# Kernel tuning notes

Hardware: AMD Instinct MI355X
Metric: run time of the kernel (lower is better)

## Reference

```python
import jax, jax.numpy as jnp
import numpy as np

EOS_IDX = 1
B, S, V, E, H = 32, 64, 32000, 512, 512


def _gru_step(x, h, w_ih, w_hh, b_ih, b_hh):
    # PyTorch GRU cell: gates ordered (r, z, n)
    gi = x @ w_ih.T + b_ih
    gh = h @ w_hh.T + b_hh
    i_r, i_z, i_n = jnp.split(gi, 3, axis=-1)
    h_r, h_z, h_n = jnp.split(gh, 3, axis=-1)
    r = jax.nn.sigmoid(i_r + h_r)
    z = jax.nn.sigmoid(i_z + h_z)
    n = jnp.tanh(i_n + r * h_n)
    return (1.0 - z) * n + z * h


def setup_inputs() -> dict:
    key = jax.random.key(0)
    ks = jax.random.split(key, 16)
    u = lambda k, shape: jax.random.uniform(k, shape, jnp.float32, -1.0, 1.0) / np.sqrt(H)
    return {
        "targets": jax.random.randint(ks[0], (B, S), 0, V),
        "targets_kws": jax.random.randint(ks[1], (B, S), 0, V),
        "sent_state": jax.random.normal(ks[2], (1, B, H), jnp.float32),
        "targets_len": jax.random.randint(ks[3], (B,), 1, S),
        "emb": jax.random.normal(ks[4], (V, E), jnp.float32) * 0.05,
        "w_ih_w": u(ks[5], (3 * H, 2 * E)),
        "w_hh_w": u(ks[6], (3 * H, H)),
        "b_ih_w": u(ks[7], (3 * H,)),
        "b_hh_w": u(ks[8], (3 * H,)),
        "w_ih_s": u(ks[9], (3 * H, H)),
        "w_hh_s": u(ks[10], (3 * H, H)),
        "b_ih_s": u(ks[11], (3 * H,)),
        "b_hh_s": u(ks[12], (3 * H,)),
        "out_w": u(ks[13], (V, H)),
        "out_b": u(ks[14], (V,)),
    }


def reference(targets, targets_kws, sent_state, targets_len,
              emb, w_ih_w, w_hh_w, b_ih_w, b_hh_w,
              w_ih_s, w_hh_s, b_ih_s, b_hh_s, out_w, out_b):
    seq = targets.shape[1]
    h0 = sent_state[0]  # nlayers = 1 -> (B, H)
    last_words = targets[:, :-1].T   # (S-1, B)
    keywords = targets_kws[:, 1:].T  # (S-1, B)
    next_words = targets[:, 1:].T    # (S-1, B)

    def step(carry, inp):
        word_h, sent_h = carry
        lw, kw, nw = inp
        x = jnp.concatenate([emb[kw], emb[lw]], axis=-1)  # (B, 2E)
        word_h = _gru_step(x, word_h, w_ih_w, w_hh_w, b_ih_w, b_hh_w)
        logp = jax.nn.log_softmax(word_h @ out_w.T + out_b, axis=-1)
        m = (nw == EOS_IDX).astype(word_h.dtype)[:, None]  # EOS mask
        tmp = _gru_step(word_h, sent_h, w_ih_s, w_hh_s, b_ih_s, b_hh_s)
        sent_h2 = sent_h * (1.0 - m) + tmp * m
        word_h2 = word_h * (1.0 - m) + tmp * m
        return (word_h2, sent_h2), logp

    _, logps = jax.lax.scan(step, (h0, h0), (last_words, keywords, next_words))
    # logps: (S-1, B, V). Masked NLL as in mask_loss().
    tok_logp = jnp.take_along_axis(logps, next_words[:, :, None], axis=2)[:, :, 0]
    valid = (targets_len[None, :] > jnp.arange(1, seq)[:, None]).astype(logps.dtype)
    return -(tok_logp * valid).sum()
```

## Files before the change

### kernel.cpp

```cpp
#include <hip/hip_runtime.h>
#include <stdint.h>

typedef short bf16x8 __attribute__((ext_vector_type(8)));
typedef float f32x4 __attribute__((ext_vector_type(4)));
typedef unsigned short u16;
typedef unsigned long long u64;

#define B_  32
#define S_  64
#define V_  32000
#define H_  512
#define T_  63
#define R_  2016
#define RP_ 2048
#define G3_ 1536
#define NWG 32

#define o_X      0ull
#define o_Wih    4194304ull
#define o_OutW   7340032ull
#define o_PackHH 40108032ull
#define o_PackIS 41680896ull
#define o_PackHS 43253760ull
#define o_GI     44826624ull
#define o_WHf    57212928ull
#define o_WHb    61341696ull
#define o_HPUB   63438848ull
#define o_SPUB   63504384ull
#define o_ARR    63569920ull
#define o_PART   63733760ull
#define o_LSE    72122368ull
#define o_RL     72130560ull
#define o_FLG    72138752ull

__device__ __forceinline__ u16 f2b(float f) {
  unsigned u = __float_as_uint(f);
  u = (u + 0x7FFFu + ((u >> 16) & 1u)) >> 16;
  return (u16)u;
}
__device__ __forceinline__ float sigm(float x) { return 1.0f / (1.0f + __expf(-x)); }

__device__ __forceinline__ void fbar(int* arr, int ph, int tid) {
  __syncthreads();
  if (tid == 0) {
    __hip_atomic_fetch_add(&arr[ph], 1, __ATOMIC_RELAXED, __HIP_MEMORY_SCOPE_AGENT);
    while (__hip_atomic_load(&arr[ph], __ATOMIC_RELAXED, __HIP_MEMORY_SCOPE_AGENT) < NWG)
      __builtin_amdgcn_s_sleep(1);
  }
  __syncthreads();
}

__global__ __launch_bounds__(256) void k_cvt(const float* __restrict__ src,
                                             u16* __restrict__ dst, int n) {
  int i4 = (blockIdx.x * 256 + threadIdx.x) * 4;
  if (i4 < n) {
    float4 v = *(const float4*)(src + i4);
    u16 t[4] = {f2b(v.x), f2b(v.y), f2b(v.z), f2b(v.w)};
    *(uint2*)(dst + i4) = *(uint2*)t;
  }
}

__global__ __launch_bounds__(256) void k_pack(const float* __restrict__ w, u16* __restrict__ up) {
  int uid = blockIdx.x * 256 + threadIdx.x;
  int lane = uid & 63;
  int ksct = uid >> 6;
  int ks = ksct & 15, ct = ksct >> 4;
  int nrow = ct * 16 + (lane & 15);
  int k0 = ks * 32 + (lane >> 4) * 8;
  const float* p = w + (size_t)nrow * 512 + k0;
  float4 v0 = *(const float4*)p;
  float4 v1 = *(const float4*)(p + 4);
  u16 t[8] = {f2b(v0.x), f2b(v0.y), f2b(v0.z), f2b(v0.w),
              f2b(v1.x), f2b(v1.y), f2b(v1.z), f2b(v1.w)};
  *(uint4*)(up + (size_t)uid * 8) = *(uint4*)t;
}

__global__ __launch_bounds__(256) void k_gather(const float* __restrict__ emb,
                                                const int* __restrict__ tg,
                                                const int* __restrict__ tk,
                                                u16* __restrict__ X) {
  int r = blockIdx.x;
  int tid = threadIdx.x;
  u16* xr = X + (size_t)r * 1024;
  if (r < R_) {
    int t = r >> 5, b = r & 31;
    int kw = tk[b * 64 + t + 1];
    int lw = tg[b * 64 + t];
    const float* src = (tid < 128) ? (emb + (size_t)kw * 512 + tid * 4)
                                   : (emb + (size_t)lw * 512 + (tid - 128) * 4);
    float4 v = *(const float4*)src;
    u16 o[4] = {f2b(v.x), f2b(v.y), f2b(v.z), f2b(v.w)};
    *(uint2*)(xr + tid * 4) = *(uint2*)o;
  } else {
    u16 z[4] = {0, 0, 0, 0};
    *(uint2*)(xr + tid * 4) = *(uint2*)z;
  }
}

__global__ __launch_bounds__(256) void k_init(const float* __restrict__ sent,
                                              const int* __restrict__ tg,
                                              u64* __restrict__ hpub, u64* __restrict__ spub,
                                              u16* __restrict__ whb, int* __restrict__ flg,
                                              int* __restrict__ arr) {
  int idx = blockIdx.x * 256 + threadIdx.x;
  whb[(size_t)R_ * 512 + idx] = 0;
  if (idx < 2048) {
    int b = idx >> 6, c = idx & 63;
    const float* p = sent + (size_t)b * 512 + c * 8;
    float4 v0 = *(const float4*)p;
    float4 v1 = *(const float4*)(p + 4);
    u16 t[8] = {f2b(v0.x), f2b(v0.y), f2b(v0.z), f2b(v0.w),
                f2b(v1.x), f2b(v1.y), f2b(v1.z), f2b(v1.w)};
    int slot = c ^ (b & 7);
    u64* d = hpub + b * 128 + slot * 2;
    d[0] = ((const u64*)t)[0];
    d[1] = ((const u64*)t)[1];
    u64* s = spub + b * 128 + slot * 2;
    s[0] = ((const u64*)t)[0];
    s[1] = ((const u64*)t)[1];
  }
  if (blockIdx.x == 0 && threadIdx.x < 63) {
    int f = 0;
    for (int b = 0; b < 32; ++b) f |= (tg[b * 64 + threadIdx.x + 1] == 1);
    flg[threadIdx.x] = f;
  }
  if (blockIdx.x == 1) arr[threadIdx.x] = 0;
}

template <int EPI>
__global__ __launch_bounds__(256) void k_gemm(const u16* __restrict__ A, const u16* __restrict__ Bw,
                                              const float* __restrict__ bias, int N, int K, int nrt,
                                              float* __restrict__ outC, int Mstore,
                                              float2* __restrict__ parts) {
  __shared__ u16 As[128 * 64];
  __shared__ u16 Bs[128 * 64];
  int bid = blockIdx.x;
  int rt = bid % nrt, ct = bid / nrt;
  int m0 = rt * 128, n0 = ct * 128;
  int tid = threadIdx.x;
  int lane = tid & 63, wid = tid >> 6;
  int wr = wid >> 1, wc = wid & 1;
  f32x4 z = {0.f, 0.f, 0.f, 0.f};
  f32x4 acc[4][4];
#pragma unroll
  for (int i = 0; i < 4; ++i)
#pragma unroll
    for (int j = 0; j < 4; ++j) acc[i][j] = z;

  int nkt = K >> 6;
  for (int kt = 0; kt < nkt; ++kt) {
    __syncthreads();
#pragma unroll
    for (int it = 0; it < 4; ++it) {
      int idx = it * 256 + tid;
      int row = idx >> 3;
      int kch = idx & 7;
      int sch = kch ^ (row & 7);
      *(uint4*)(&As[row * 64 + kch * 8]) =
          *(const uint4*)(A + (size_t)(m0 + row) * K + kt * 64 + sch * 8);
      *(uint4*)(&Bs[row * 64 + kch * 8]) =
          *(const uint4*)(Bw + (size_t)(n0 + row) * K + kt * 64 + sch * 8);
    }
    __syncthreads();
#pragma unroll
    for (int kk = 0; kk < 2; ++kk) {
      bf16x8 af[4], bf[4];
#pragma unroll
      for (int i = 0; i < 4; ++i) {
        int row = wr * 64 + i * 16 + (lane & 15);
        int c = kk * 4 + (lane >> 4);
        af[i] = *(const bf16x8*)(&As[row * 64 + ((c ^ (row & 7)) * 8)]);
      }
#pragma unroll
      for (int j = 0; j < 4; ++j) {
        int row = wc * 64 + j * 16 + (lane & 15);
        int c = kk * 4 + (lane >> 4);
        bf[j] = *(const bf16x8*)(&Bs[row * 64 + ((c ^ (row & 7)) * 8)]);
      }
#pragma unroll
      for (int i = 0; i < 4; ++i)
#pragma unroll
        for (int j = 0; j < 4; ++j)
          acc[i][j] = __builtin_amdgcn_mfma_f32_16x16x32_bf16(af[i], bf[j], acc[i][j], 0, 0, 0);
    }
  }

  if (EPI == 0) {
#pragma unroll
    for (int i = 0; i < 4; ++i) {
      int mb = m0 + wr * 64 + i * 16 + ((lane >> 4) << 2);
#pragma unroll
      for (int j = 0; j < 4; ++j) {
        int n = n0 + wc * 64 + j * 16 + (lane & 15);
        float bb = bias[n];
#pragma unroll
        for (int r = 0; r < 4; ++r) {
          int m = mb + r;
          if (m < Mstore) outC[(size_t)m * N + n] = acc[i][j][r] + bb;
        }
      }
    }
  } else {
    float bb[4];
#pragma unroll
    for (int j = 0; j < 4; ++j) bb[j] = bias[n0 + wc * 64 + j * 16 + (lane & 15)];
    int chunk = ct * 2 + wc;
#pragma unroll
    for (int i = 0; i < 4; ++i) {
#pragma unroll
      for (int r = 0; r < 4; ++r) {
        float l0 = acc[i][0][r] + bb[0], l1 = acc[i][1][r] + bb[1];
        float l2 = acc[i][2][r] + bb[2], l3 = acc[i][3][r] + bb[3];
        float mx = fmaxf(fmaxf(l0, l1), fmaxf(l2, l3));
#pragma unroll
        for (int d = 1; d < 16; d <<= 1) mx = fmaxf(mx, __shfl_xor(mx, d));
        float s = __expf(l0 - mx) + __expf(l1 - mx) + __expf(l2 - mx) + __expf(l3 - mx);
#pragma unroll
        for (int d = 1; d < 16; d <<= 1) s += __shfl_xor(s, d);
        if ((lane & 15) == 0) {
          int m = m0 + wr * 64 + i * 16 + ((lane >> 4) << 2) + r;
          parts[(size_t)m * 512 + chunk] = make_float2(mx, s);
        }
      }
    }
  }
}

__device__ __forceinline__ f32x4 mm16_lds(const u16* hb, const u16* bl, int lane, int rt) {
  f32x4 a0 = {0.f, 0.f, 0.f, 0.f}, a1 = {0.f, 0.f, 0.f, 0.f};
  int row = rt * 16 + (lane & 15);
  int cb = lane >> 4;
#pragma unroll
  for (int ks = 0; ks < 16; ks += 2) {
    int c0 = ks * 4 + cb, c1 = c0 + 4;
    bf16x8 av0 = *(const bf16x8*)(&hb[row * 512 + ((c0 ^ (row & 7)) * 8)]);
    bf16x8 bv0 = *(const bf16x8*)(&bl[(ks * 64 + lane) * 8]);
    bf16x8 av1 = *(const bf16x8*)(&hb[row * 512 + ((c1 ^ (row & 7)) * 8)]);
    bf16x8 bv1 = *(const bf16x8*)(&bl[((ks + 1) * 64 + lane) * 8]);
    a0 = __builtin_amdgcn_mfma_f32_16x16x32_bf16(av0, bv0, a0, 0, 0, 0);
    a1 = __builtin_amdgcn_mfma_f32_16x16x32_bf16(av1, bv1, a1, 0, 0, 0);
  }
  return a0 + a1;
}

__device__ __forceinline__ f32x4 mm16g(const u16* hb, const u16* bp, int lane, int rt) {
  f32x4 acc = {0.f, 0.f, 0.f, 0.f};
#pragma unroll
  for (int ks = 0; ks < 16; ++ks) {
    int row = rt * 16 + (lane & 15);
    int c = ks * 4 + (lane >> 4);
    bf16x8 a = *(const bf16x8*)(&hb[row * 512 + ((c ^ (row & 7)) * 8)]);
    bf16x8 b = *(const bf16x8*)(bp + (size_t)(ks * 64 + lane) * 8);
    acc = __builtin_amdgcn_mfma_f32_16x16x32_bf16(a, b, acc, 0, 0, 0);
  }
  return acc;
}

__global__ __launch_bounds__(512) void k_recur(
    const float* __restrict__ gi, const u16* __restrict__ packHH, const u16* __restrict__ packIS,
    const u16* __restrict__ packHS, const float* __restrict__ bhh_w, const float* __restrict__ bih_s,
    const float* __restrict__ bhh_s, const int* __restrict__ targets, const int* __restrict__ flags,
    const float* __restrict__ sent, u64* __restrict__ hpub, u64* __restrict__ spub,
    float* __restrict__ whf, u16* __restrict__ whb, int* __restrict__ arr) {
  __shared__ u16 hb[32 * 512];
  __shared__ u16 wls[3 * 1024 * 8];
  __shared__ float ghl[6][32][16];
  __shared__ float gil[2][3][32][16];
  __shared__ float hloc[32][16];
  __shared__ float sloc[32][16];
  __shared__ u16 hps[32][16];
  __shared__ u16 sps[32][16];

  const int tid = threadIdx.x;
  const int lane = tid & 63;
  const int wid = tid >> 6;
  const int gate = wid >> 1;
  const int rt = wid & 1;
  const int g = blockIdx.x;
  const int b_ = tid >> 4, hl = tid & 15;
  const int n_ = g * 16 + hl;

  {
    const uint4* src = (const uint4*)packHH;
    uint4* dst = (uint4*)wls;
    for (int lin = tid; lin < 3072; lin += 512) {
      int which = lin >> 10, off = lin & 1023;
      dst[lin] = src[(size_t)(which * 32 + g) * 1024 + off];
    }
  }
  {
    float v = sent[(size_t)b_ * 512 + n_];
    hloc[b_][hl] = v;
    sloc[b_][hl] = v;
  }
  if (wid >= 6) {
    int lid = tid - 384;
    const float* base = gi + (size_t)g * 16;
#pragma unroll
    for (int q = 0; q < 3; ++q) {
      int fid = q * 128 + lid;
      int ga = fid >> 7, rem = fid & 127;
      int b = rem >> 2, h4 = (rem & 3) << 2;
      *(float4*)&gil[0][ga][b][h4] = *(const float4*)(base + (size_t)b * 1536 + ga * 512 + h4);
    }
  }
  const float bw_r = bhh_w[n_], bw_z = bhh_w[512 + n_], bw_n = bhh_w[1024 + n_];
  __syncthreads();

  int ph = 0;
  int scur = 0;
  for (int t = 0; t < T_; ++t) {
    const int cur = t & 1, nxt = cur ^ 1;
    {
      const u64* src = hpub + cur * 4096;
      u64* d = (u64*)hb;
      for (int idx = tid; idx < 4096; idx += 512)
        d[idx] = __hip_atomic_load(&src[idx], __ATOMIC_RELAXED, __HIP_MEMORY_SCOPE_AGENT);
    }
    __syncthreads();
    if (wid < 6) {
      f32x4 acc = mm16_lds(hb, wls + gate * 8192, lane, rt);
      int bb = rt * 16 + ((lane >> 4) << 2);
      int cl = lane & 15;
#pragma unroll
      for (int r4 = 0; r4 < 4; ++r4) ghl[gate][bb + r4][cl] = acc[r4];
    } else if (t + 1 < T_) {
      int lid = tid - 384;
      const float* base = gi + (size_t)(t + 1) * 32 * 1536 + g * 16;
#pragma unroll
      for (int q = 0; q < 3; ++q) {
        int fid = q * 128 + lid;
        int ga = fid >> 7, rem = fid & 127;
        int b = rem >> 2, h4 = (rem & 3) << 2;
        *(float4*)&gil[nxt][ga][b][h4] = *(const float4*)(base + (size_t)b * 1536 + ga * 512 + h4);
      }
    }
    __syncthreads();
    {
      int rrow = t * 32 + b_;
      float r_ = sigm(gil[cur][0][b_][hl] + ghl[0][b_][hl] + bw_r);
      float z_ = sigm(gil[cur][1][b_][hl] + ghl[1][b_][hl] + bw_z);
      float nn = tanhf(gil[cur][2][b_][hl] + r_ * (ghl[2][b_][hl] + bw_n));
      float hold = hloc[b_][hl];
      float hnew = (1.f - z_) * nn + z_ * hold;
      hloc[b_][hl] = hnew;
      u16 h16 = f2b(hnew);
      hps[b_][hl] = h16;
      whf[(size_t)rrow * 512 + n_] = hnew;
      whb[(size_t)rrow * 512 + n_] = h16;
    }
    __syncthreads();
    if (tid < 128) {
      int b = tid >> 2, j = tid & 3, q = j >> 1, half = j & 1;
      u64 v = *(const u64*)&hps[b][q * 8 + half * 4];
      int slot = (2 * g + q) ^ (b & 7);
      __hip_atomic_store(&hpub[nxt * 4096 + b * 128 + slot * 2 + half], v,
                         __ATOMIC_RELAXED, __HIP_MEMORY_SCOPE_AGENT);
    }
    fbar(arr, ph, tid); ++ph;

    if (flags[t]) {
      {
        const u64* src = hpub + nxt * 4096;
        u64* d = (u64*)hb;
        for (int idx = tid; idx < 4096; idx += 512)
          d[idx] = __hip_atomic_load(&src[idx], __ATOMIC_RELAXED, __HIP_MEMORY_SCOPE_AGENT);
      }
      fbar(arr, ph, tid); ++ph;
      f32x4 ax = {0.f, 0.f, 0.f, 0.f};
      if (wid < 6) ax = mm16g(hb, packIS + (size_t)(gate * 32 + g) * 8192, lane, rt);
      __syncthreads();
      {
        const u64* src = spub + scur * 4096;
        u64* d = (u64*)hb;
        for (int idx = tid; idx < 4096; idx += 512)
          d[idx] = __hip_atomic_load(&src[idx], __ATOMIC_RELAXED, __HIP_MEMORY_SCOPE_AGENT);
      }
      __syncthreads();
      if (wid < 6) {
        f32x4 ah = mm16g(hb, packHS + (size_t)(gate * 32 + g) * 8192, lane, rt);
        int bb = rt * 16 + ((lane >> 4) << 2);
        int cl = lane & 15;
#pragma unroll
        for (int r4 = 0; r4 < 4; ++r4) {
          ghl[gate][bb + r4][cl] = ax[r4];
          ghl[3 + gate][bb + r4][cl] = ah[r4];
        }
      }
      __syncthreads();
      {
        float r_ = sigm(ghl[0][b_][hl] + bih_s[n_] + ghl[3][b_][hl] + bhh_s[n_]);
        float z_ = sigm(ghl[1][b_][hl] + bih_s[512 + n_] + ghl[4][b_][hl] + bhh_s[512 + n_]);
        float nn = tanhf(ghl[2][b_][hl] + bih_s[1024 + n_] +
                         r_ * (ghl[5][b_][hl] + bhh_s[1024 + n_]));
        float hs = sloc[b_][hl];
        float tmpv = (1.f - z_) * nn + z_ * hs;
        int m = (targets[b_ * 64 + t + 1] == 1);
        float hw = hloc[b_][hl];
        float hw2 = m ? tmpv : hw;
        float hs2 = m ? tmpv : hs;
        hloc[b_][hl] = hw2;
        sloc[b_][hl] = hs2;
        hps[b_][hl] = f2b(hw2);
        sps[b_][hl] = f2b(hs2);
      }
      __syncthreads();
      if (tid < 128) {
        int b = tid >> 2, j = tid & 3, q = j >> 1, half = j & 1;
        int slot = (2 * g + q) ^ (b & 7);
        u64 v = *(const u64*)&hps[b][q * 8 + half * 4];
        __hip_atomic_store(&hpub[nxt * 4096 + b * 128 + slot * 2 + half], v,
                           __ATOMIC_RELAXED, __HIP_MEMORY_SCOPE_AGENT);
        u64 w = *(const u64*)&sps[b][q * 8 + half * 4];
        __hip_atomic_store(&spub[(scur ^ 1) * 4096 + b * 128 + slot * 2 + half], w,
                           __ATOMIC_RELAXED, __HIP_MEMORY_SCOPE_AGENT);
      }
      scur ^= 1;
      fbar(arr, ph, tid); ++ph;
    }
  }
}

__global__ __launch_bounds__(256) void k_lse(const float2* __restrict__ parts,
                                             float* __restrict__ lse) {
  int wid = threadIdx.x >> 6, lane = threadIdx.x & 63;
  int row = blockIdx.x * 4 + wid;
  if (row >= R_) return;
  float m = -3.0e38f, s = 0.f;
  for (int c = lane; c < 500; c += 64) {
    float2 p = parts[(size_t)row * 512 + c];
    float nm = fmaxf(m, p.x);
    s = s * __expf(m - nm) + p.y * __expf(p.x - nm);
    m = nm;
  }
#pragma unroll
  for (int d = 1; d < 64; d <<= 1) {
    float om = __shfl_xor(m, d), os = __shfl_xor(s, d);
    float nm = fmaxf(m, om);
    s = s * __expf(m - nm) + os * __expf(om - nm);
    m = nm;
  }
  if (lane == 0) lse[row] = m + __logf(s);
}

__global__ __launch_bounds__(256) void k_rowloss(const float* __restrict__ whf,
                                                 const float* __restrict__ outw,
                                                 const float* __restrict__ outb,
                                                 const int* __restrict__ targets,
                                                 const int* __restrict__ tlen,
                                                 const float* __restrict__ lse,
                                                 float* __restrict__ rl) {
  int wid = threadIdx.x >> 6, lane = threadIdx.x & 63;
  int r = blockIdx.x * 4 + wid;
  if (r >= R_) return;
  int t = r >> 5, b = r & 31;
  int nw = targets[b * 64 + t + 1];
  const float* hv = whf + (size_t)r * 512;
  const float* wv = outw + (size_t)nw * 512;
  float acc = 0.f;
#pragma unroll
  for (int q = 0; q < 2; ++q) {
    int k = lane * 8 + q * 4;
    float4 a = *(const float4*)(hv + k);
    float4 w = *(const float4*)(wv + k);
    acc += a.x * w.x + a.y * w.y + a.z * w.z + a.w * w.w;
  }
#pragma unroll
  for (int d = 1; d < 64; d <<= 1) acc += __shfl_xor(acc, d);
  if (lane == 0) {
    bool valid = tlen[b] > (t + 1);
    rl[r] = valid ? (lse[r] - (acc + outb[nw])) : 0.f;
  }
}

__global__ __launch_bounds__(256) void k_sum(const float* __restrict__ rl, float* __restrict__ out) {
  __shared__ float sm[256];
  float a = 0.f;
  for (int i = threadIdx.x; i < R_; i += 256) a += rl[i];
  sm[threadIdx.x] = a;
  __syncthreads();
  for (int s = 128; s > 0; s >>= 1) {
    if (threadIdx.x < s) sm[threadIdx.x] += sm[threadIdx.x + s];
    __syncthreads();
  }
  if (threadIdx.x == 0) out[0] = sm[0];
}

extern "C" void kernel_launch(void* const* d_in, const int* in_sizes, int n_in,
                              void* d_out, int out_size, void* d_ws, size_t ws_size,
                              hipStream_t stream) {
  const int* targets = (const int*)d_in[0];
  const int* tkws    = (const int*)d_in[1];
  const float* sent  = (const float*)d_in[2];
  const int* tlen    = (const int*)d_in[3];
  const float* emb   = (const float*)d_in[4];
  const float* wihw  = (const float*)d_in[5];
  const float* whhw  = (const float*)d_in[6];
  const float* bihw  = (const float*)d_in[7];
  const float* bhhw  = (const float*)d_in[8];
  const float* wihs  = (const float*)d_in[9];
  const float* whhs  = (const float*)d_in[10];
  const float* bihs  = (const float*)d_in[11];
  const float* bhhs  = (const float*)d_in[12];
  const float* outw  = (const float*)d_in[13];
  const float* outb  = (const float*)d_in[14];
  float* out = (float*)d_out;
  char* ws = (char*)d_ws;

  u16* X       = (u16*)(ws + o_X);
  u16* Wih16   = (u16*)(ws + o_Wih);
  u16* OutW16  = (u16*)(ws + o_OutW);
  u16* PackHH  = (u16*)(ws + o_PackHH);
  u16* PackIS  = (u16*)(ws + o_PackIS);
  u16* PackHS  = (u16*)(ws + o_PackHS);
  float* GI    = (float*)(ws + o_GI);
  float* WHf   = (float*)(ws + o_WHf);
  u16* WHb     = (u16*)(ws + o_WHb);
  u64* HPUB    = (u64*)(ws + o_HPUB);
  u64* SPUB    = (u64*)(ws + o_SPUB);
  int* ARR     = (int*)(ws + o_ARR);
  float2* PART = (float2*)(ws + o_PART);
  float* LSE   = (float*)(ws + o_LSE);
  float* RL    = (float*)(ws + o_RL);
  int* FLG     = (int*)(ws + o_FLG);

  k_cvt<<<dim3(16000), dim3(256), 0, stream>>>(outw, OutW16, V_ * H_);
  k_cvt<<<dim3(1536), dim3(256), 0, stream>>>(wihw, Wih16, G3_ * 1024);
  k_pack<<<dim3(384), dim3(256), 0, stream>>>(whhw, PackHH);
  k_pack<<<dim3(384), dim3(256), 0, stream>>>(wihs, PackIS);
  k_pack<<<dim3(384), dim3(256), 0, stream>>>(whhs, PackHS);
  k_gather<<<dim3(RP_), dim3(256), 0, stream>>>(emb, targets, tkws, X);
  k_init<<<dim3(64), dim3(256), 0, stream>>>(sent, targets, HPUB, SPUB, WHb, FLG, ARR);

  k_gemm<0><<<dim3(16 * 12), dim3(256), 0, stream>>>(X, Wih16, bihw, G3_, 1024, 16, GI, R_, nullptr);

  k_recur<<<dim3(NWG), dim3(512), 0, stream>>>(GI, PackHH, PackIS, PackHS, bhhw, bihs, bhhs,
                                               targets, FLG, sent, HPUB, SPUB, WHf, WHb, ARR);

  k_gemm<1><<<dim3(16 * 250), dim3(256), 0, stream>>>(WHb, OutW16, outb, V_, 512, 16, nullptr, 0, PART);

  k_lse<<<dim3(504), dim3(256), 0, stream>>>(PART, LSE);
  k_rowloss<<<dim3(504), dim3(256), 0, stream>>>(WHf, outw, outb, targets, tlen, LSE, RL);
  k_sum<<<dim3(1), dim3(256), 0, stream>>>(RL, out);
}
```

Baseline: 427.4 us.

## Overlap output-projection GEMM with GRU recurrence in one persistent mega kernel

Merges the recurrent GRU kernel and the vocabulary-projection GEMM with fused partial softmax into a single launch. 32 workgroups run the sequential recurrence and publish a step counter after each timestep. 192 extra workgroups loop over 128x128 output tiles and spin until the hidden-state rows they need are ready. The goal is to hide the large logits GEMM behind the latency-bound recurrence instead of running them back to back. The worker blocks share the GPU with the recurrence blocks, so they can slow its barriers through contention, and the design relies on all workgroups being co-resident.

After: 413.3 us. 3.3% less time.

```diff
diff --git a/kernel.cpp b/kernel.cpp
--- a/kernel.cpp
+++ b/kernel.cpp
@@ -15,6 +15,8 @@
 #define RP_ 2048
 #define G3_ 1536
 #define NWG 32
+#define NWORK 192
+#define NTILE 4000
 
 #define o_X      0ull
 #define o_Wih    4194304ull
@@ -28,6 +30,7 @@
 #define o_HPUB   63438848ull
 #define o_SPUB   63504384ull
 #define o_ARR    63569920ull
+#define o_CTR    63571968ull
 #define o_PART   63733760ull
 #define o_LSE    72122368ull
 #define o_RL     72130560ull
@@ -101,7 +104,7 @@
                                               const int* __restrict__ tg,
                                               u64* __restrict__ hpub, u64* __restrict__ spub,
                                               u16* __restrict__ whb, int* __restrict__ flg,
-                                              int* __restrict__ arr) {
+                                              int* __restrict__ arr, int* __restrict__ ctr) {
   int idx = blockIdx.x * 256 + threadIdx.x;
   whb[(size_t)R_ * 512 + idx] = 0;
   if (idx < 2048) {
@@ -125,13 +128,12 @@
     flg[threadIdx.x] = f;
   }
   if (blockIdx.x == 1) arr[threadIdx.x] = 0;
-}
-
-template <int EPI>
-__global__ __launch_bounds__(256) void k_gemm(const u16* __restrict__ A, const u16* __restrict__ Bw,
-                                              const float* __restrict__ bias, int N, int K, int nrt,
-                                              float* __restrict__ outC, int Mstore,
-                                              float2* __restrict__ parts) {
+  if (blockIdx.x == 2) ctr[threadIdx.x] = 0;
+}
+
+__global__ __launch_bounds__(256) void k_gemm0(const u16* __restrict__ A, const u16* __restrict__ Bw,
+                                               const float* __restrict__ bias, int N, int K, int nrt,
+                                               float* __restrict__ outC, int Mstore) {
   __shared__ u16 As[128 * 64];
   __shared__ u16 Bs[128 * 64];
   int bid = blockIdx.x;
@@ -184,47 +186,40 @@
           acc[i][j] = __builtin_amdgcn_mfma_f32_16x16x32_bf16(af[i], bf[j], acc[i][j], 0, 0, 0);
     }
   }
-
-  if (EPI == 0) {
-#pragma unroll
-    for (int i = 0; i < 4; ++i) {
-      int mb = m0 + wr * 64 + i * 16 + ((lane >> 4) << 2);
-#pragma unroll
-      for (int j = 0; j < 4; ++j) {
-        int n = n0 + wc * 64 + j * 16 + (lane & 15);
-        float bb = bias[n];
-#pragma unroll
-        for (int r = 0; r < 4; ++r) {
-          int m = mb + r;
-          if (m < Mstore) outC[(size_t)m * N + n] = acc[i][j][r] + bb;
-        }
-      }
-    }
-  } else {
-    float bb[4];
-#pragma unroll
-    for (int j = 0; j < 4; ++j) bb[j] = bias[n0 + wc * 64 + j * 16 + (lane & 15)];
-    int chunk = ct * 2 + wc;
-#pragma unroll
-    for (int i = 0; i < 4; ++i) {
+#pragma unroll
+  for (int i = 0; i < 4; ++i) {
+    int mb = m0 + wr * 64 + i * 16 + ((lane >> 4) << 2);
+#pragma unroll
+    for (int j = 0; j < 4; ++j) {
+      int n = n0 + wc * 64 + j * 16 + (lane & 15);
+      float bb = bias[n];
 #pragma unroll
       for (int r = 0; r < 4; ++r) {
-        float l0 = acc[i][0][r] + bb[0], l1 = acc[i][1][r] + bb[1];
-        float l2 = acc[i][2][r] + bb[2], l3 = acc[i][3][r] + bb[3];
-        float mx = fmaxf(fmaxf(l0, l1), fmaxf(l2, l3));
-#pragma unroll
-        for (int d = 1; d < 16; d <<= 1) mx = fmaxf(mx, __shfl_xor(mx, d));
-        float s = __expf(l0 - mx) + __expf(l1 - mx) + __expf(l2 - mx) + __expf(l3 - mx);
-#pragma unroll
-        for (int d = 1; d < 16; d <<= 1) s += __shfl_xor(s, d);
-        if ((lane & 15) == 0) {
-          int m = m0 + wr * 64 + i * 16 + ((lane >> 4) << 2) + r;
-          parts[(size_t)m * 512 + chunk] = make_float2(mx, s);
-        }
-      }
-    }
-  }
-}
+        int m = mb + r;
+        if (m < Mstore) outC[(size_t)m * N + n] = acc[i][j][r] + bb;
+      }
+    }
+  }
+}
+
+struct RecurSM {
+  u16 hb[32 * 512];
+  u16 wls[3 * 1024 * 8];
+  float ghl[6][32][16];
+  float gil[2][3][32][16];
+  float hloc[32][16];
+  float sloc[32][16];
+  u16 hps[32][16];
+  u16 sps[32][16];
+};
+struct GemmSM {
+  u16 As[128 * 64];
+  u16 Bs[128 * 64];
+};
+union MegaSM {
+  RecurSM r;
+  GemmSM g;
+};
 
 __device__ __forceinline__ f32x4 mm16_lds(const u16* hb, const u16* bl, int lane, int rt) {
   f32x4 a0 = {0.f, 0.f, 0.f, 0.f}, a1 = {0.f, 0.f, 0.f, 0.f};
@@ -256,22 +251,109 @@
   return acc;
 }
 
-__global__ __launch_bounds__(512) void k_recur(
+__device__ __forceinline__ void gemm_tile(u16* As, u16* Bs, const u16* __restrict__ A,
+                                          const u16* __restrict__ Bw,
+                                          const float* __restrict__ bias,
+                                          int rt, int ct, float2* __restrict__ parts, int tid) {
+  int m0 = rt * 128, n0 = ct * 128;
+  int lane = tid & 63, wid = tid >> 6;
+  int wr = wid >> 1, wc = wid & 1;
+  f32x4 z = {0.f, 0.f, 0.f, 0.f};
+  f32x4 acc[2][4];
+#pragma unroll
+  for (int i = 0; i < 2; ++i)
+#pragma unroll
+    for (int j = 0; j < 4; ++j) acc[i][j] = z;
+
+  for (int kt = 0; kt < 8; ++kt) {
+    __syncthreads();
+#pragma unroll
+    for (int it = 0; it < 2; ++it) {
+      int idx = it * 512 + tid;
+      int row = idx >> 3, kch = idx & 7;
+      *(uint4*)(&As[row * 64 + kch * 8]) =
+          *(const uint4*)(A + (size_t)(m0 + row) * 512 + kt * 64 + kch * 8);
+      int sch = kch ^ (row & 7);
+      *(uint4*)(&Bs[row * 64 + kch * 8]) =
+          *(const uint4*)(Bw + (size_t)(n0 + row) * 512 + kt * 64 + sch * 8);
+    }
+    __syncthreads();
+#pragma unroll
+    for (int kk = 0; kk < 2; ++kk) {
+      bf16x8 af[2], bf[4];
+#pragma unroll
+      for (int i = 0; i < 2; ++i) {
+        int row = wr * 32 + i * 16 + (lane & 15);
+        int c = kk * 4 + (lane >> 4);
+        af[i] = *(const bf16x8*)(&As[row * 64 + ((c ^ (row & 7)) * 8)]);
+      }
+#pragma unroll
+      for (int j = 0; j < 4; ++j) {
+        int row = wc * 64 + j * 16 + (lane & 15);
+        int c = kk * 4 + (lane >> 4);
+        bf[j] = *(const bf16x8*)(&Bs[row * 64 + ((c ^ (row & 7)) * 8)]);
+      }
+#pragma unroll
+      for (int i = 0; i < 2; ++i)
+#pragma unroll
+        for (int j = 0; j < 4; ++j)
+          acc[i][j] = __builtin_amdgcn_mfma_f32_16x16x32_bf16(af[i], bf[j], acc[i][j], 0, 0, 0);
+    }
+  }
+  float bb[4];
+#pragma unroll
+  for (int j = 0; j < 4; ++j) bb[j] = bias[n0 + wc * 64 + j * 16 + (lane & 15)];
+  int chunk = ct * 2 + wc;
+#pragma unroll
+  for (int i = 0; i < 2; ++i) {
+#pragma unroll
+    for (int r = 0; r < 4; ++r) {
+      float l0 = acc[i][0][r] + bb[0], l1 = acc[i][1][r] + bb[1];
+      float l2 = acc[i][2][r] + bb[2], l3 = acc[i][3][r] + bb[3];
+      float mx = fmaxf(fmaxf(l0, l1), fmaxf(l2, l3));
+#pragma unroll
+      for (int d = 1; d < 16; d <<= 1) mx = fmaxf(mx, __shfl_xor(mx, d));
+      float s = __expf(l0 - mx) + __expf(l1 - mx) + __expf(l2 - mx) + __expf(l3 - mx);
+#pragma unroll
+      for (int d = 1; d < 16; d <<= 1) s += __shfl_xor(s, d);
+      if ((lane & 15) == 0) {
+        int m = m0 + wr * 32 + i * 16 + ((lane >> 4) << 2) + r;
+        parts[(size_t)m * 512 + chunk] = make_float2(mx, s);
+      }
+    }
+  }
+}
+
+__global__ __launch_bounds__(512) void k_mega(
     const float* __restrict__ gi, const u16* __restrict__ packHH, const u16* __restrict__ packIS,
     const u16* __restrict__ packHS, const float* __restrict__ bhh_w, const float* __restrict__ bih_s,
     const float* __restrict__ bhh_s, const int* __restrict__ targets, const int* __restrict__ flags,
     const float* __restrict__ sent, u64* __restrict__ hpub, u64* __restrict__ spub,
-    float* __restrict__ whf, u16* __restrict__ whb, int* __restrict__ arr) {
-  __shared__ u16 hb[32 * 512];
-  __shared__ u16 wls[3 * 1024 * 8];
-  __shared__ float ghl[6][32][16];
-  __shared__ float gil[2][3][32][16];
-  __shared__ float hloc[32][16];
-  __shared__ float sloc[32][16];
-  __shared__ u16 hps[32][16];
-  __shared__ u16 sps[32][16];
-
+    float* __restrict__ whf, u16* __restrict__ whb, int* __restrict__ arr, int* __restrict__ ctr,
+    const u16* __restrict__ outw16, const float* __restrict__ outb, float2* __restrict__ parts) {
+  __shared__ MegaSM sm;
   const int tid = threadIdx.x;
+  int* steps = ctr + 32;
+
+  if (blockIdx.x >= NWG) {
+    const int w = blockIdx.x - NWG;
+    for (int k = 0;; ++k) {
+      int tile = w + k * NWORK;
+      if (tile >= NTILE) break;
+      int rt = tile / 250;
+      int ct = tile - rt * 250;
+      if (tid == 0) {
+        int need = 4 * rt + 4;
+        if (need > T_) need = T_;
+        while (__hip_atomic_load(steps, __ATOMIC_ACQUIRE, __HIP_MEMORY_SCOPE_AGENT) < need)
+          __builtin_amdgcn_s_sleep(64);
+      }
+      gemm_tile(sm.g.As, sm.g.Bs, whb, outw16, outb, rt, ct, parts, tid);
+      __syncthreads();
+    }
+    return;
+  }
+
   const int lane = tid & 63;
   const int wid = tid >> 6;
   const int gate = wid >> 1;
@@ -282,7 +364,7 @@
 
   {
     const uint4* src = (const uint4*)packHH;
-    uint4* dst = (uint4*)wls;
+    uint4* dst = (uint4*)sm.r.wls;
     for (int lin = tid; lin < 3072; lin += 512) {
       int which = lin >> 10, off = lin & 1023;
       dst[lin] = src[(size_t)(which * 32 + g) * 1024 + off];
@@ -290,8 +372,8 @@
   }
   {
     float v = sent[(size_t)b_ * 512 + n_];
-    hloc[b_][hl] = v;
-    sloc[b_][hl] = v;
+    sm.r.hloc[b_][hl] = v;
+    sm.r.sloc[b_][hl] = v;
   }
   if (wid >= 6) {
     int lid = tid - 384;
@@ -301,7 +383,7 @@
       int fid = q * 128 + lid;
       int ga = fid >> 7, rem = fid & 127;
       int b = rem >> 2, h4 = (rem & 3) << 2;
-      *(float4*)&gil[0][ga][b][h4] = *(const float4*)(base + (size_t)b * 1536 + ga * 512 + h4);
+      *(float4*)&sm.r.gil[0][ga][b][h4] = *(const float4*)(base + (size_t)b * 1536 + ga * 512 + h4);
     }
   }
   const float bw_r = bhh_w[n_], bw_z = bhh_w[512 + n_], bw_n = bhh_w[1024 + n_];
@@ -313,17 +395,17 @@
     const int cur = t & 1, nxt = cur ^ 1;
     {
       const u64* src = hpub + cur * 4096;
-      u64* d = (u64*)hb;
+      u64* d = (u64*)sm.r.hb;
       for (int idx = tid; idx < 4096; idx += 512)
         d[idx] = __hip_atomic_load(&src[idx], __ATOMIC_RELAXED, __HIP_MEMORY_SCOPE_AGENT);
     }
     __syncthreads();
     if (wid < 6) {
-      f32x4 acc = mm16_lds(hb, wls + gate * 8192, lane, rt);
+      f32x4 acc = mm16_lds(sm.r.hb, sm.r.wls + gate * 8192, lane, rt);
       int bb = rt * 16 + ((lane >> 4) << 2);
       int cl = lane & 15;
 #pragma unroll
-      for (int r4 = 0; r4 < 4; ++r4) ghl[gate][bb + r4][cl] = acc[r4];
+      for (int r4 = 0; r4 < 4; ++r4) sm.r.ghl[gate][bb + r4][cl] = acc[r4];
     } else if (t + 1 < T_) {
       int lid = tid - 384;
       const float* base = gi + (size_t)(t + 1) * 32 * 1536 + g * 16;
@@ -332,87 +414,95 @@
         int fid = q * 128 + lid;
         int ga = fid >> 7, rem = fid & 127;
         int b = rem >> 2, h4 = (rem & 3) << 2;
-        *(float4*)&gil[nxt][ga][b][h4] = *(const float4*)(base + (size_t)b * 1536 + ga * 512 + h4);
+        *(float4*)&sm.r.gil[nxt][ga][b][h4] =
+            *(const float4*)(base + (size_t)b * 1536 + ga * 512 + h4);
       }
     }
     __syncthreads();
     {
       int rrow = t * 32 + b_;
-      float r_ = sigm(gil[cur][0][b_][hl] + ghl[0][b_][hl] + bw_r);
-      float z_ = sigm(gil[cur][1][b_][hl] + ghl[1][b_][hl] + bw_z);
-      float nn = tanhf(gil[cur][2][b_][hl] + r_ * (ghl[2][b_][hl] + bw_n));
-      float hold = hloc[b_][hl];
+      float r_ = sigm(sm.r.gil[cur][0][b_][hl] + sm.r.ghl[0][b_][hl] + bw_r);
+      float z_ = sigm(sm.r.gil[cur][1][b_][hl] + sm.r.ghl[1][b_][hl] + bw_z);
+      float nn = tanhf(sm.r.gil[cur][2][b_][hl] + r_ * (sm.r.ghl[2][b_][hl] + bw_n));
+      float hold = sm.r.hloc[b_][hl];
       float hnew = (1.f - z_) * nn + z_ * hold;
-      hloc[b_][hl] = hnew;
-      u16 h16 = f2b(hnew);
-      hps[b_][hl] = h16;
+      sm.r.hloc[b_][hl] = hnew;
+      sm.r.hps[b_][hl] = f2b(hnew);
       whf[(size_t)rrow * 512 + n_] = hnew;
-      whb[(size_t)rrow * 512 + n_] = h16;
     }
     __syncthreads();
     if (tid < 128) {
       int b = tid >> 2, j = tid & 3, q = j >> 1, half = j & 1;
-      u64 v = *(const u64*)&hps[b][q * 8 + half * 4];
+      u64 v = *(const u64*)&sm.r.hps[b][q * 8 + half * 4];
       int slot = (2 * g + q) ^ (b & 7);
       __hip_atomic_store(&hpub[nxt * 4096 + b * 128 + slot * 2 + half], v,
                          __ATOMIC_RELAXED, __HIP_MEMORY_SCOPE_AGENT);
+    } else if (tid < 256) {
+      int l = tid - 128;
+      int b = l >> 2, j = l & 3, q = j >> 1, half = j & 1;
+      u64 v = *(const u64*)&sm.r.hps[b][q * 8 + half * 4];
+      int slot = (2 * g + q) ^ (b & 7);
+      __hip_atomic_store((u64*)whb + (size_t)(t * 32 + b) * 128 + slot * 2 + half, v,
+                         __ATOMIC_RELAXED, __HIP_MEMORY_SCOPE_AGENT);
     }
     fbar(arr, ph, tid); ++ph;
+    if (g == 0 && tid == 0)
+      __hip_atomic_store(steps, t + 1, __ATOMIC_RELEASE, __HIP_MEMORY_SCOPE_AGENT);
 
     if (flags[t]) {
       {
         const u64* src = hpub + nxt * 4096;
-        u64* d = (u64*)hb;
+        u64* d = (u64*)sm.r.hb;
         for (int idx = tid; idx < 4096; idx += 512)
           d[idx] = __hip_atomic_load(&src[idx], __ATOMIC_RELAXED, __HIP_MEMORY_SCOPE_AGENT);
       }
       fbar(arr, ph, tid); ++ph;
       f32x4 ax = {0.f, 0.f, 0.f, 0.f};
-      if (wid < 6) ax = mm16g(hb, packIS + (size_t)(gate * 32 + g) * 8192, lane, rt);
+      if (wid < 6) ax = mm16g(sm.r.hb, packIS + (size_t)(gate * 32 + g) * 8192, lane, rt);
       __syncthreads();
       {
         const u64* src = spub + scur * 4096;
-        u64* d = (u64*)hb;
+        u64* d = (u64*)sm.r.hb;
         for (int idx = tid; idx < 4096; idx += 512)
           d[idx] = __hip_atomic_load(&src[idx], __ATOMIC_RELAXED, __HIP_MEMORY_SCOPE_AGENT);
       }
       __syncthreads();
       if (wid < 6) {
-        f32x4 ah = mm16g(hb, packHS + (size_t)(gate * 32 + g) * 8192, lane, rt);
+        f32x4 ah = mm16g(sm.r.hb, packHS + (size_t)(gate * 32 + g) * 8192, lane, rt);
         int bb = rt * 16 + ((lane >> 4) << 2);
         int cl = lane & 15;
 #pragma unroll
         for (int r4 = 0; r4 < 4; ++r4) {
-          ghl[gate][bb + r4][cl] = ax[r4];
-          ghl[3 + gate][bb + r4][cl] = ah[r4];
+          sm.r.ghl[gate][bb + r4][cl] = ax[r4];
+          sm.r.ghl[3 + gate][bb + r4][cl] = ah[r4];
         }
       }
       __syncthreads();
       {
-        float r_ = sigm(ghl[0][b_][hl] + bih_s[n_] + ghl[3][b_][hl] + bhh_s[n_]);
-        float z_ = sigm(ghl[1][b_][hl] + bih_s[512 + n_] + ghl[4][b_][hl] + bhh_s[512 + n_]);
-        float nn = tanhf(ghl[2][b_][hl] + bih_s[1024 + n_] +
-                         r_ * (ghl[5][b_][hl] + bhh_s[1024 + n_]));
-        float hs = sloc[b_][hl];
+        float r_ = sigm(sm.r.ghl[0][b_][hl] + bih_s[n_] + sm.r.ghl[3][b_][hl] + bhh_s[n_]);
+        float z_ = sigm(sm.r.ghl[1][b_][hl] + bih_s[512 + n_] + sm.r.ghl[4][b_][hl] + bhh_s[512 + n_]);
+        float nn = tanhf(sm.r.ghl[2][b_][hl] + bih_s[1024 + n_] +
+                         r_ * (sm.r.ghl[5][b_][hl] + bhh_s[1024 + n_]));
+        float hs = sm.r.sloc[b_][hl];
         float tmpv = (1.f - z_) * nn + z_ * hs;
         int m = (targets[b_ * 64 + t + 1] == 1);
-        float hw = hloc[b_][hl];
+        float hw = sm.r.hloc[b_][hl];
         float hw2 = m ? tmpv : hw;
         float hs2 = m ? tmpv : hs;
-        hloc[b_][hl] = hw2;
-        sloc[b_][hl] = hs2;
-        hps[b_][hl] = f2b(hw2);
-        sps[b_][hl] = f2b(hs2);
+        sm.r.hloc[b_][hl] = hw2;
+        sm.r.sloc[b_][hl] = hs2;
+        sm.r.hps[b_][hl] = f2b(hw2);
+        sm.r.sps[b_][hl] = f2b(hs2);
       }
       __syncthreads();
       if (tid < 128) {
         int b = tid >> 2, j = tid & 3, q = j >> 1, half = j & 1;
         int slot = (2 * g + q) ^ (b & 7);
-        u64 v = *(const u64*)&hps[b][q * 8 + half * 4];
+        u64 v = *(const u64*)&sm.r.hps[b][q * 8 + half * 4];
         __hip_atomic_store(&hpub[nxt * 4096 + b * 128 + slot * 2 + half], v,
                            __ATOMIC_RELAXED, __HIP_MEMORY_SCOPE_AGENT);
-        u64 w = *(const u64*)&sps[b][q * 8 + half * 4];
-        __hip_atomic_store(&spub[(scur ^ 1) * 4096 + b * 128 + slot * 2 + half], w,
+        u64 w2 = *(const u64*)&sm.r.sps[b][q * 8 + half * 4];
+        __hip_atomic_store(&spub[(scur ^ 1) * 4096 + b * 128 + slot * 2 + half], w2,
                            __ATOMIC_RELAXED, __HIP_MEMORY_SCOPE_AGENT);
       }
       scur ^= 1;
@@ -519,6 +609,7 @@
   u64* HPUB    = (u64*)(ws + o_HPUB);
   u64* SPUB    = (u64*)(ws + o_SPUB);
   int* ARR     = (int*)(ws + o_ARR);
+  int* CTR     = (int*)(ws + o_CTR);
   float2* PART = (float2*)(ws + o_PART);
   float* LSE   = (float*)(ws + o_LSE);
   float* RL    = (float*)(ws + o_RL);
@@ -530,14 +621,13 @@
   k_pack<<<dim3(384), dim3(256), 0, stream>>>(wihs, PackIS);
   k_pack<<<dim3(384), dim3(256), 0, stream>>>(whhs, PackHS);
   k_gather<<<dim3(RP_), dim3(256), 0, stream>>>(emb, targets, tkws, X);
-  k_init<<<dim3(64), dim3(256), 0, stream>>>(sent, targets, HPUB, SPUB, WHb, FLG, ARR);
-
-  k_gemm<0><<<dim3(16 * 12), dim3(256), 0, stream>>>(X, Wih16, bihw, G3_, 1024, 16, GI, R_, nullptr);
-
-  k_recur<<<dim3(NWG), dim3(512), 0, stream>>>(GI, PackHH, PackIS, PackHS, bhhw, bihs, bhhs,
-                                               targets, FLG, sent, HPUB, SPUB, WHf, WHb, ARR);
-
-  k_gemm<1><<<dim3(16 * 250), dim3(256), 0, stream>>>(WHb, OutW16, outb, V_, 512, 16, nullptr, 0, PART);
+  k_init<<<dim3(64), dim3(256), 0, stream>>>(sent, targets, HPUB, SPUB, WHb, FLG, ARR, CTR);
+
+  k_gemm0<<<dim3(16 * 12), dim3(256), 0, stream>>>(X, Wih16, bihw, G3_, 1024, 16, GI, R_);
+
+  k_mega<<<dim3(NWG + NWORK), dim3(512), 0, stream>>>(GI, PackHH, PackIS, PackHS, bhhw, bihs, bhhs,
+                                                      targets, FLG, sent, HPUB, SPUB, WHf, WHb,
+                                                      ARR, CTR, OutW16, outb, PART);
 
   k_lse<<<dim3(504), dim3(256), 0, stream>>>(PART, LSE);
   k_rowloss<<<dim3(504), dim3(256), 0, stream>>>(WHf, outw, outb, targets, tlen, LSE, RL);
```
